# Kernel tuning notes

Hardware: AMD Instinct MI355X
Metric: run time of the kernel (lower is better)

## Reference

```python
import jax, jax.numpy as jnp
import numpy as np

B, IC, OC, K, H, W = 8, 512, 512, 3, 32, 32
GAIN, LRMUL = 1.0, 1.0
# compute_runtime_coef: fan_in = prod(weight_shape[:-1])
RC_CONV = GAIN / np.sqrt(K * K * IC) * LRMUL   # conv weight [K,K,IC,OC]
RC_DENSE = GAIN / np.sqrt(IC) * LRMUL          # dense weight [IC, IC]


def setup_inputs() -> dict:
    key = jax.random.key(0)
    ks = jax.random.split(key, 4)
    x = jax.random.normal(ks[0], (B, IC, H, W), dtype=jnp.float32)
    w = jax.random.normal(ks[1], (B, IC), dtype=jnp.float32)
    # init_std = 1/lrmul = 1.0 for both weights; bias init zeros
    conv_w = jax.random.normal(ks[2], (K, K, IC, OC), dtype=jnp.float32)
    dense_w = jax.random.normal(ks[3], (IC, IC), dtype=jnp.float32)
    dense_b = jnp.zeros((IC,), dtype=jnp.float32)
    return {"x": x, "w": w, "conv_w": conv_w, "dense_w": dense_w, "dense_b": dense_b}


def reference(x, w, conv_w, dense_w, dense_b):
    b, ic, h, wd = x.shape
    # modulation: style = Dense(w) + bias + 1
    style = w @ (RC_DENSE * dense_w) + LRMUL * dense_b + 1.0        # [B, IC]
    wt = (RC_CONV * conv_w)[None] * style[:, None, None, :, None]   # [B,K,K,IC,OC]
    # demodulation: rsqrt of sum of squares over (kh, kw, ic)
    d = jax.lax.rsqrt(jnp.sum(jnp.square(wt), axis=(1, 2, 3)) + 1e-8)  # [B, OC]
    wt = wt * d[:, None, None, None, :]
    # grouped conv with groups = batch: weight -> OIHW [B*OC, IC, K, K]
    w_g = jnp.transpose(wt, (0, 4, 3, 1, 2)).reshape(b * OC, ic, K, K)
    xg = x.reshape(1, b * ic, h, wd)
    y = jax.lax.conv_general_dilated(
        xg, w_g, window_strides=(1, 1), padding="SAME",
        dimension_numbers=("NCHW", "OIHW", "NCHW"), feature_group_count=b)
    return y.reshape(b, OC, h, wd)
```

## Files before the change

### kernel.cpp

```cpp
#include <hip/hip_runtime.h>
#include <stdint.h>


#define B_   8
#define IC_  512
#define OC_  512

static constexpr float RC_DENSE = 0.04419417382415922f;
static constexpr float RC_CONV  = 0.014731391274719739f;

typedef _Float16 half8    __attribute__((ext_vector_type(8)));
typedef float    floatx16 __attribute__((ext_vector_type(16)));

__device__ __forceinline__ void g2l(const void* g, void* l) {
  __builtin_amdgcn_global_load_lds(
      (const __attribute__((address_space(1))) void*)g,
      (__attribute__((address_space(3))) void*)l, 16, 0, 0);
}

__global__ __launch_bounds__(256) void style_kernel(
    const float* __restrict__ wv, const float* __restrict__ dw,
    const float* __restrict__ db, float* __restrict__ sm,
    float* __restrict__ sm2) {
  const int b = blockIdx.y;
  const int i = blockIdx.x * 64 + (threadIdx.x & 63);
  const int jg = threadIdx.x >> 6;
  __shared__ float red[4][64];
  float p = 0.f;
  for (int j = jg * 128; j < jg * 128 + 128; ++j)
    p += wv[b * IC_ + j] * dw[(size_t)j * IC_ + i];
  red[jg][threadIdx.x & 63] = p;
  __syncthreads();
  if (threadIdx.x < 64) {
    float s = red[0][threadIdx.x] + red[1][threadIdx.x] +
              red[2][threadIdx.x] + red[3][threadIdx.x];
    s = s * RC_DENSE + db[i] + 1.0f;
    float v = s * RC_CONV;
    sm[b * IC_ + i] = v;
    sm2[b * IC_ + i] = v * v;
  }
}

__global__ __launch_bounds__(256) void prep_kernel(
    const float* __restrict__ cw, const float* __restrict__ x,
    const float* __restrict__ sm, const float* __restrict__ sm2,
    _Float16* __restrict__ Wtf, float* __restrict__ dpart,
    _Float16* __restrict__ xsp) {
  __shared__ __align__(16) char smem[33280];
  const int bid = blockIdx.x;
  const int tid = threadIdx.x;
  if (bid < 256) {
    _Float16* LA = (_Float16*)smem;
    float* redall = (float*)(smem + 18432);
    const int by2 = bid >> 4, icb = bid & 15;
    const int by = by2 >> 1, h2 = by2 & 1;
    const int oc0 = by * 64 + h2 * 32, ic0 = icb * 32;
    const int ocl = tid & 31, g = tid >> 5;
    float sq4[4] = {};
    for (int m = 0; m < 36; ++m) {
      int r = m * 8 + g;
      int t = r >> 5, icl = r & 31;
      float v = cw[(size_t)(t * IC_ + ic0 + icl) * OC_ + oc0 + ocl];
      sq4[m & 3] += v * v;
      LA[m * 256 + ocl * 8 + g] = (_Float16)v;
    }
    for (int b = 0; b < 8; ++b) {
      float p = 0.f;
      for (int s = 0; s < 4; ++s)
        p += sm2[b * IC_ + ic0 + g + 8 * s] * sq4[s];
      redall[(b * 8 + g) * 32 + ocl] = p;
    }
    __syncthreads();
    _Float16* dst = Wtf + (size_t)(by * 16 + icb) * 18432;
    for (int it = 0; it < 5; ++it) {
      int c = it * 256 + tid;
      if (c < 1152) {
        int m = c >> 5, o2 = c & 31;
        *(half8*)(dst + (size_t)(m * 64 + h2 * 32 + o2) * 8) =
            *(const half8*)&LA[m * 256 + o2 * 8];
      }
    }
    const int bb = tid >> 5, o3 = tid & 31;
    float s = 0.f;
    for (int g2 = 0; g2 < 8; ++g2) s += redall[(bb * 8 + g2) * 32 + o3];
    dpart[(size_t)icb * 4096 + bb * OC_ + oc0 + o3] = s;
  } else {
    _Float16* Xt = (_Float16*)smem;
    const int rb = bid - 256;
    const int b = rb >> 5, h = rb & 31;
    for (int k = 0; k < 16; ++k) {
      int idx = k * 256 + tid;
      int ic = idx >> 3, wc = (idx & 7) * 4;
      float4 v = *(const float4*)&x[((size_t)(b * IC_ + ic) * 32 + h) * 32 + wc];
      float s = sm[b * IC_ + ic];
      Xt[(wc + 0) * 520 + ic] = (_Float16)(v.x * s);
      Xt[(wc + 1) * 520 + ic] = (_Float16)(v.y * s);
      Xt[(wc + 2) * 520 + ic] = (_Float16)(v.z * s);
      Xt[(wc + 3) * 520 + ic] = (_Float16)(v.w * s);
    }
    __syncthreads();
    _Float16* xb = xsp + (size_t)b * 16 * 36992;
    const int r = h + 1;
    half8 z = {};
    for (int it = 0; it < 9; ++it) {
      int c = it * 256 + tid;
      if (c < 2176) {
        int icb = c / 136, rem = c - 136 * icb, kkq = rem / 34, C = rem - 34 * kkq;
        half8 val = z;
        if (C != 0 && C != 33)
          val = *(const half8*)&Xt[(C - 1) * 520 + icb * 32 + kkq * 8];
        *(half8*)&xb[(size_t)icb * 36992 + (size_t)r * 1088 + kkq * 272 + C * 8] = val;
      }
    }
    if (h == 0 || h == 31) {
      const int rz = (h == 0) ? 0 : 33;
      for (int it = 0; it < 9; ++it) {
        int c = it * 256 + tid;
        if (c < 2176) {
          int icb = c / 136, rem = c - 136 * icb, kkq = rem / 34, C = rem - 34 * kkq;
          *(half8*)&xb[(size_t)icb * 36992 + (size_t)rz * 1088 + kkq * 272 + C * 8] = z;
        }
      }
    }
  }
}


#define VM10 asm volatile("s_waitcnt vmcnt(10)" ::: "memory")
#define VM5  asm volatile("s_waitcnt vmcnt(5)" ::: "memory")
#define VM0  asm volatile("s_waitcnt vmcnt(0)" ::: "memory")
#define VMNONE ((void)0)

#define PHASE(KK, SH, PAR, DO_A, G2L_STMT, VM_STMT)                          \
  {                                                                          \
    if (DO_A) {                                                              \
      const _Float16* Ad = dyn + ((KK) * 2 + (PAR)) * 9216 +                 \
                           kq * 512 + wm * 256 + n * 8;                      \
      _Pragma("unroll")                                                      \
      for (int t_ = 0; t_ < 9; ++t_)                                         \
        av[t_] = *(const half8*)(Ad + (t_ * 2) * 512);                       \
    }                                                                        \
    const _Float16* Xd = XB + ((KK) * 2 + (PAR)) * 5440 +                    \
                         (2 * wn + 2 * (SH)) * 544 + kq * 272 + n * 8;       \
    half8 xv0[3], xv1[3];                                                    \
    _Pragma("unroll")                                                        \
    for (int kw_ = 0; kw_ < 3; ++kw_) {                                      \
      xv0[kw_] = *(const half8*)(Xd + kw_ * 8);                              \
      xv1[kw_] = *(const half8*)(Xd + 544 + kw_ * 8);                        \
    }                                                                        \
    G2L_STMT;                                                                \
    __builtin_amdgcn_s_barrier();                                            \
    asm volatile("s_waitcnt lgkmcnt(0)" ::: "memory");                       \
    __builtin_amdgcn_sched_barrier(0);                                       \
    __builtin_amdgcn_s_setprio(1);                                           \
    _Pragma("unroll")                                                        \
    for (int kw_ = 0; kw_ < 3; ++kw_) {                                      \
      if (SH == 0) {                                                         \
        acc[0] = __builtin_amdgcn_mfma_f32_32x32x16_f16(av[0 + kw_], xv0[kw_], acc[0], 0, 0, 0); \
        acc[1] = __builtin_amdgcn_mfma_f32_32x32x16_f16(av[0 + kw_], xv1[kw_], acc[1], 0, 0, 0); \
        acc[0] = __builtin_amdgcn_mfma_f32_32x32x16_f16(av[3 + kw_], xv1[kw_], acc[0], 0, 0, 0); \
      } else {                                                               \
        acc[1] = __builtin_amdgcn_mfma_f32_32x32x16_f16(av[3 + kw_], xv0[kw_], acc[1], 0, 0, 0); \
        acc[0] = __builtin_amdgcn_mfma_f32_32x32x16_f16(av[6 + kw_], xv0[kw_], acc[0], 0, 0, 0); \
        acc[1] = __builtin_amdgcn_mfma_f32_32x32x16_f16(av[6 + kw_], xv1[kw_], acc[1], 0, 0, 0); \
      }                                                                      \
    }                                                                        \
    __builtin_amdgcn_s_setprio(0);                                           \
    __builtin_amdgcn_sched_barrier(0);                                       \
    VM_STMT;                                                                 \
    __builtin_amdgcn_s_barrier();                                            \
  }

__global__ __launch_bounds__(512, 1) void conv_kernel(
    const _Float16* __restrict__ Wtf,
    const _Float16* __restrict__ xsp,
    const float* __restrict__ dpart,
    float* __restrict__ out) {
  extern __shared__ __align__(16) _Float16 dyn[];
  _Float16* XB = dyn + 36864;
  float* redd = (float*)(dyn + 58624);
  float* dvl  = redd + 512;

  const int by = blockIdx.x, bx = blockIdx.y, b = blockIdx.z;
  const int tid = threadIdx.x, lane = tid & 63, w = tid >> 6;
  const int wm = w & 1, wn = w >> 1;
  const int n = lane & 31, kq = lane >> 5;
  const int h0 = bx * 8;

  const _Float16* gA = Wtf + (size_t)(by * 16) * 18432;
  const _Float16* gX = xsp + (size_t)b * 16 * 36992 + (size_t)h0 * 1088;

  auto stageA3 = [&](int g) {
    const int icb = g >> 1, kk = g & 1, par = icb & 1;
    const _Float16* a = gA + (size_t)icb * 18432;
    _Float16* Ad = dyn + (kk * 2 + par) * 9216;
#pragma unroll
    for (int k = 0; k < 2; ++k) {
      int c = w * 144 + k * 64 + lane;
      int mi = c >> 6, o = c & 63;
      int m = (mi >> 1) * 4 + kk * 2 + (mi & 1);
      g2l(a + (size_t)(m * 512 + o * 8), Ad + c * 8);
    }
    {
      int c = w * 144 + 128 + lane;
      if (lane < 16) {
        int mi = c >> 6, o = c & 63;
        int m = (mi >> 1) * 4 + kk * 2 + (mi & 1);
        g2l(a + (size_t)(m * 512 + o * 8), Ad + c * 8);
      }
    }
  };
  auto stageX2 = [&](int g) {
    const int icb = g >> 1, kk = g & 1, par = icb & 1;
    const _Float16* xg = gX + (size_t)icb * 36992 + kk * 544;
    _Float16* Xd = XB + (kk * 2 + par) * 5440;
    {
      int c = w * 85 + lane;
      int r = c / 68, o = c - r * 68;
      g2l(xg + (size_t)(r * 1088 + o * 8), Xd + c * 8);
    }
    {
      int c = w * 85 + 64 + lane;
      if (lane < 21) {
        int r = c / 68, o = c - r * 68;
        g2l(xg + (size_t)(r * 1088 + o * 8), Xd + c * 8);
      }
    }
  };

  floatx16 acc[2] = {};
  half8 av[9];
  stageA3(0); stageX2(0);
  stageA3(1); stageX2(1);
  stageA3(2); stageX2(2);
  VM10;
  __builtin_amdgcn_s_barrier();

  for (int st = 0; st < 14; ++st) {
    const int par = st & 1;
    const int g3 = 2 * st + 3, g4 = 2 * st + 4;
    PHASE(0, 0, par, true,  stageA3(g3), VMNONE)
    PHASE(0, 1, par, false, stageX2(g3), VM10)
    PHASE(1, 0, par, true,  stageA3(g4), VMNONE)
    PHASE(1, 1, par, false, stageX2(g4), VM10)
  }
  PHASE(0, 0, 0, true,  stageA3(31), VMNONE)
  PHASE(0, 1, 0, false, stageX2(31), VM10)
  PHASE(1, 0, 0, true,  VMNONE, VMNONE)
  PHASE(1, 1, 0, false, VMNONE, VM5)
  PHASE(0, 0, 1, true,  VMNONE, VMNONE)
  PHASE(0, 1, 1, false, VMNONE, VM0)
  PHASE(1, 0, 1, true,  VMNONE, VMNONE)
  PHASE(1, 1, 1, false, VMNONE, VMNONE)

  const int oc0 = by * 64 + wm * 32;
  __syncthreads();
  {
    const int oc_l = tid & 63, ig = tid >> 6;
    float s = dpart[(size_t)(ig * 2) * 4096 + b * OC_ + by * 64 + oc_l] +
              dpart[(size_t)(ig * 2 + 1) * 4096 + b * OC_ + by * 64 + oc_l];
    redd[ig * 64 + oc_l] = s;
  }
  __syncthreads();
  if (tid < 64) {
    float s = 1e-8f;
#pragma unroll
    for (int g = 0; g < 8; ++g) s += redd[g * 64 + tid];
    dvl[tid] = rsqrtf(s);
  }
  __syncthreads();
  const int r0 = h0 + 2 * wn;
#pragma unroll
  for (int rg = 0; rg < 16; ++rg) {
    const int row = (rg & 3) + 8 * (rg >> 2) + 4 * kq;
    const float dv = dvl[wm * 32 + row];
    float* op = out + ((size_t)b * OC_ + oc0 + row) * 1024 + r0 * 32 + n;
    op[0]  = acc[0][rg] * dv;
    op[32] = acc[1][rg] * dv;
  }
}

extern "C" void kernel_launch(void* const* d_in, const int* in_sizes, int n_in,
                              void* d_out, int out_size, void* d_ws, size_t ws_size,
                              hipStream_t stream) {
  const float* x       = (const float*)d_in[0];
  const float* w       = (const float*)d_in[1];
  const float* conv_w  = (const float*)d_in[2];
  const float* dense_w = (const float*)d_in[3];
  const float* dense_b = (const float*)d_in[4];
  float* out = (float*)d_out;

  char* ws = (char*)d_ws;
  float*    sm    = (float*)ws;
  float*    sm2   = (float*)(ws + (16 << 10));
  float*    dpart = (float*)(ws + (32 << 10));
  _Float16* Wtf   = (_Float16*)(ws + (288 << 10));
  _Float16* xsp   = (_Float16*)(ws + (288 << 10) + 4718592);

  static int dyn_set = 0;
  if (!dyn_set) {
    hipFuncSetAttribute((const void*)conv_kernel,
                        hipFuncAttributeMaxDynamicSharedMemorySize, 119552);
    dyn_set = 1;
  }

  style_kernel<<<dim3(8, B_), 256, 0, stream>>>(w, dense_w, dense_b, sm, sm2);
  prep_kernel<<<512, 256, 0, stream>>>(conv_w, x, sm, sm2, Wtf, dpart, xsp);
  conv_kernel<<<dim3(8, 4, B_), 512, 119552, stream>>>(Wtf, xsp, dpart, out);
}
```

Measured before the change: 127.5 us.

## Double-buffer LDS-to-register fragments to overlap reads with MFMA

Splits the per-phase LDS reads into separate A and X fragment loads and double-buffers them in registers (avA/avB, xvA/xvB), so the next phase's operands are read while the current phase's MFMAs run. Full lgkmcnt(0) waits are replaced by partial lgkmcnt counts, and the vmcnt waits are rebalanced. This adds substantial register pressure and relies on exact wait-count accounting across the rearranged global-to-LDS staging barriers.

```diff
diff --git a/kernel.cpp b/kernel.cpp
--- a/kernel.cpp
+++ b/kernel.cpp
@@ -127,44 +127,58 @@
 
 
 #define VM10 asm volatile("s_waitcnt vmcnt(10)" ::: "memory")
-#define VM5  asm volatile("s_waitcnt vmcnt(5)" ::: "memory")
-#define VM0  asm volatile("s_waitcnt vmcnt(0)" ::: "memory")
+#define VM8  asm volatile("s_waitcnt vmcnt(8)"  ::: "memory")
+#define VM5  asm volatile("s_waitcnt vmcnt(5)"  ::: "memory")
+#define VM0  asm volatile("s_waitcnt vmcnt(0)"  ::: "memory")
+#define LG15 asm volatile("s_waitcnt lgkmcnt(15)" ::: "memory")
+#define LG6  asm volatile("s_waitcnt lgkmcnt(6)"  ::: "memory")
+#define LG0  asm volatile("s_waitcnt lgkmcnt(0)"  ::: "memory")
 #define VMNONE ((void)0)
 
-#define PHASE(KK, SH, PAR, DO_A, G2L_STMT, VM_STMT)                          \
+#define LOADX(XV, KK, SH, PAR)                                               \
   {                                                                          \
-    if (DO_A) {                                                              \
-      const _Float16* Ad = dyn + ((KK) * 2 + (PAR)) * 9216 +                 \
-                           kq * 512 + wm * 256 + n * 8;                      \
-      _Pragma("unroll")                                                      \
-      for (int t_ = 0; t_ < 9; ++t_)                                         \
-        av[t_] = *(const half8*)(Ad + (t_ * 2) * 512);                       \
-    }                                                                        \
-    const _Float16* Xd = XB + ((KK) * 2 + (PAR)) * 5440 +                    \
-                         (2 * wn + 2 * (SH)) * 544 + kq * 272 + n * 8;       \
-    half8 xv0[3], xv1[3];                                                    \
+    const _Float16* Xd_ = XB + ((KK) * 2 + (PAR)) * 5440 +                   \
+                          (2 * wn + 2 * (SH)) * 544 + kq * 272 + n * 8;      \
     _Pragma("unroll")                                                        \
     for (int kw_ = 0; kw_ < 3; ++kw_) {                                      \
-      xv0[kw_] = *(const half8*)(Xd + kw_ * 8);                              \
-      xv1[kw_] = *(const half8*)(Xd + 544 + kw_ * 8);                        \
+      XV##0[kw_] = *(const half8*)(Xd_ + kw_ * 8);                           \
+      XV##1[kw_] = *(const half8*)(Xd_ + 544 + kw_ * 8);                     \
     }                                                                        \
-    G2L_STMT;                                                                \
-    __builtin_amdgcn_s_barrier();                                            \
-    asm volatile("s_waitcnt lgkmcnt(0)" ::: "memory");                       \
-    __builtin_amdgcn_sched_barrier(0);                                       \
-    __builtin_amdgcn_s_setprio(1);                                           \
+  }
+#define LOADA(AV, KK, PAR)                                                   \
+  {                                                                          \
+    const _Float16* Ad_ = dyn + ((KK) * 2 + (PAR)) * 9216 +                  \
+                          kq * 512 + wm * 256 + n * 8;                       \
+    _Pragma("unroll")                                                        \
+    for (int t_ = 0; t_ < 9; ++t_)                                           \
+      AV[t_] = *(const half8*)(Ad_ + (t_ * 2) * 512);                        \
+  }
+
+#define MFMA9(AV, XV, SH)                                                    \
     _Pragma("unroll")                                                        \
     for (int kw_ = 0; kw_ < 3; ++kw_) {                                      \
       if (SH == 0) {                                                         \
-        acc[0] = __builtin_amdgcn_mfma_f32_32x32x16_f16(av[0 + kw_], xv0[kw_], acc[0], 0, 0, 0); \
-        acc[1] = __builtin_amdgcn_mfma_f32_32x32x16_f16(av[0 + kw_], xv1[kw_], acc[1], 0, 0, 0); \
-        acc[0] = __builtin_amdgcn_mfma_f32_32x32x16_f16(av[3 + kw_], xv1[kw_], acc[0], 0, 0, 0); \
+        acc[0] = __builtin_amdgcn_mfma_f32_32x32x16_f16(AV[0 + kw_], XV##0[kw_], acc[0], 0, 0, 0); \
+        acc[1] = __builtin_amdgcn_mfma_f32_32x32x16_f16(AV[0 + kw_], XV##1[kw_], acc[1], 0, 0, 0); \
+        acc[0] = __builtin_amdgcn_mfma_f32_32x32x16_f16(AV[3 + kw_], XV##1[kw_], acc[0], 0, 0, 0); \
       } else {                                                               \
-        acc[1] = __builtin_amdgcn_mfma_f32_32x32x16_f16(av[3 + kw_], xv0[kw_], acc[1], 0, 0, 0); \
-        acc[0] = __builtin_amdgcn_mfma_f32_32x32x16_f16(av[6 + kw_], xv0[kw_], acc[0], 0, 0, 0); \
-        acc[1] = __builtin_amdgcn_mfma_f32_32x32x16_f16(av[6 + kw_], xv1[kw_], acc[1], 0, 0, 0); \
+        acc[1] = __builtin_amdgcn_mfma_f32_32x32x16_f16(AV[3 + kw_], XV##0[kw_], acc[1], 0, 0, 0); \
+        acc[0] = __builtin_amdgcn_mfma_f32_32x32x16_f16(AV[6 + kw_], XV##0[kw_], acc[0], 0, 0, 0); \
+        acc[1] = __builtin_amdgcn_mfma_f32_32x32x16_f16(AV[6 + kw_], XV##1[kw_], acc[1], 0, 0, 0); \
       }                                                                      \
-    }                                                                        \
+    }
+
+#define PHASE(AV, XV, SH, LOADS_STMT, G2L_STMT, LG_STMT, VM_STMT)            \
+  {                                                                          \
+    __builtin_amdgcn_sched_barrier(0);                                       \
+    LOADS_STMT;                                                              \
+    __builtin_amdgcn_sched_barrier(0);                                       \
+    G2L_STMT;                                                                \
+    __builtin_amdgcn_s_barrier();                                            \
+    LG_STMT;                                                                 \
+    __builtin_amdgcn_sched_barrier(0);                                       \
+    __builtin_amdgcn_s_setprio(1);                                           \
+    MFMA9(AV, XV, SH)                                                        \
     __builtin_amdgcn_s_setprio(0);                                           \
     __builtin_amdgcn_sched_barrier(0);                                       \
     VM_STMT;                                                                 \
@@ -229,29 +243,36 @@
   };
 
   floatx16 acc[2] = {};
-  half8 av[9];
+  half8 avA[9], avB[9];
+  half8 xvA0[3], xvA1[3], xvB0[3], xvB1[3];
+
   stageA3(0); stageX2(0);
   stageA3(1); stageX2(1);
   stageA3(2); stageX2(2);
   VM10;
   __builtin_amdgcn_s_barrier();
+  LOADA(avA, 0, 0)
+  LOADX(xvA, 0, 0, 0)
+  __builtin_amdgcn_sched_barrier(0);
 
   for (int st = 0; st < 14; ++st) {
-    const int par = st & 1;
+    const int par = st & 1, nxt = par ^ 1;
     const int g3 = 2 * st + 3, g4 = 2 * st + 4;
-    PHASE(0, 0, par, true,  stageA3(g3), VMNONE)
-    PHASE(0, 1, par, false, stageX2(g3), VM10)
-    PHASE(1, 0, par, true,  stageA3(g4), VMNONE)
-    PHASE(1, 1, par, false, stageX2(g4), VM10)
-  }
-  PHASE(0, 0, 0, true,  stageA3(31), VMNONE)
-  PHASE(0, 1, 0, false, stageX2(31), VM10)
-  PHASE(1, 0, 0, true,  VMNONE, VMNONE)
-  PHASE(1, 1, 0, false, VMNONE, VM5)
-  PHASE(0, 0, 1, true,  VMNONE, VMNONE)
-  PHASE(0, 1, 1, false, VMNONE, VM0)
-  PHASE(1, 0, 1, true,  VMNONE, VMNONE)
-  PHASE(1, 1, 1, false, VMNONE, VMNONE)
+    PHASE(avA, xvA, 0, LOADX(xvB, 0, 1, par), stageA3(g3), LG6, VM8)
+    PHASE(avA, xvB, 1, LOADA(avB, 1, par); LOADX(xvA, 1, 0, par),
+          stageX2(g3), LG15, VMNONE)
+    PHASE(avB, xvA, 0, LOADX(xvB, 1, 1, par), stageA3(g4), LG6, VM8)
+    PHASE(avB, xvB, 1, LOADA(avA, 0, nxt); LOADX(xvA, 0, 0, nxt),
+          stageX2(g4), LG15, VMNONE)
+  }
+  PHASE(avA, xvA, 0, LOADX(xvB, 0, 1, 0), stageA3(31), LG6, VM8)
+  PHASE(avA, xvB, 1, LOADA(avB, 1, 0); LOADX(xvA, 1, 0, 0), stageX2(31), LG15, VMNONE)
+  PHASE(avB, xvA, 0, LOADX(xvB, 1, 1, 0), VMNONE, LG6, VM5)
+  PHASE(avB, xvB, 1, LOADA(avA, 0, 1); LOADX(xvA, 0, 0, 1), VMNONE, LG15, VMNONE)
+  PHASE(avA, xvA, 0, LOADX(xvB, 0, 1, 1), VMNONE, LG6, VM0)
+  PHASE(avA, xvB, 1, LOADA(avB, 1, 1); LOADX(xvA, 1, 0, 1), VMNONE, LG15, VMNONE)
+  PHASE(avB, xvA, 0, LOADX(xvB, 1, 1, 1), VMNONE, LG6, VMNONE)
+  PHASE(avB, xvB, 1, VMNONE, VMNONE, LG0, VMNONE)
 
   const int oc0 = by * 64 + wm * 32;
   __syncthreads();
```

Result: no change. 127.1 us (-0.3%).
